# Performance work log

Measured on AMD Instinct MI355X. Metric: run time of the kernel, lower is better.

The kernel has to match this reference:

```python
import jax, jax.numpy as jnp
import numpy as np

B, C, H, W = 2, 64, 48, 48
NH = 8
EPS = 1e-5


def conv2d(x, w, b=None, pad=0):
    out = jax.lax.conv_general_dilated(x, w, (1, 1), [(pad, pad), (pad, pad)],
                                       dimension_numbers=('NCHW', 'OIHW', 'NCHW'))
    return out if b is None else out + b[None, :, None, None]


def bn2d(x, g, b, m, v):
    # eval-mode BatchNorm2d with running stats
    return (x - m[None, :, None, None]) * (g / jnp.sqrt(v + EPS))[None, :, None, None] + b[None, :, None, None]


def ln(x, g, b):
    mu = x.mean(-1, keepdims=True)
    var = ((x - mu) ** 2).mean(-1, keepdims=True)
    return (x - mu) / jnp.sqrt(var + EPS) * g + b


def _forward(x, y, pconv_w, pconv_b, bnd_g, bnd_b, bnd_m, bnd_v,
             lnx_g, lnx_b, lny_g, lny_b, lnz_g, lnz_b,
             k_w, k_b, qv_w, qv_b, proj_w, proj_b,
             c2w1, c2b1, c2bn1_g, c2bn1_b, c2bn1_m, c2bn1_v,
             c2w2, c2b2, c2bn2_g, c2bn2_b, c2bn2_m, c2bn2_v,
             bn2_g, bn2_b, bn2_m, bn2_v,
             f1w, fbn1_g, fbn1_b, fbn1_m, fbn1_v,
             f2w, fbn2_g, fbn2_b, fbn2_m, fbn2_v,
             f3w, f3b):
    Bq, Cq, Hq, Wq = x.shape
    N = Hq * Wq
    hd = Cq // NH
    scale = hd ** -0.5
    xy = conv2d(jnp.concatenate([x, y], 1), pconv_w, pconv_b, pad=0)
    xb = bn2d(x, bnd_g, bnd_b, bnd_m, bnd_v)
    yb = bn2d(y, bnd_g, bnd_b, bnd_m, bnd_v)
    xyb = bn2d(xy, bnd_g, bnd_b, bnd_m, bnd_v)
    sc1 = xb.reshape(Bq, Cq, N).transpose(0, 2, 1)  # [B,N,C]
    sd1 = yb.reshape(Bq, Cq, N).transpose(0, 2, 1)
    xl = ln(sc1, lnx_g, lnx_b)
    yl = ln(sd1, lny_g, lny_b)
    zl = ln(xyb.reshape(Bq, Cq, N).transpose(0, 2, 1), lnz_g, lnz_b)

    def qv_heads(t):
        qv = (t @ qv_w.T + qv_b).reshape(Bq, N, 2, NH, hd)
        return qv[:, :, 0].transpose(0, 2, 1, 3), qv[:, :, 1].transpose(0, 2, 1, 3)

    x_q, x_v = qv_heads(xl)
    y_q, y_v = qv_heads(yl)
    k = (zl @ k_w.T + k_b).reshape(Bq, N, NH, hd).transpose(0, 2, 1, 3)  # [B,H,N,hd]
    attn1 = jnp.einsum('bhnd,bhmd->bhnm', x_q, k) * scale
    attn2 = jnp.einsum('bhnd,bhmd->bhnm', y_q, k) * scale
    attn = jax.nn.softmax(attn1 * attn2, axis=-1)  # product of two score maps
    xo = jnp.einsum('bhnm,bhmd->bhnd', attn, x_v).transpose(0, 2, 1, 3).reshape(Bq, N, Cq) @ proj_w.T + proj_b
    yo = jnp.einsum('bhnm,bhmd->bhnd', attn, y_v).transpose(0, 2, 1, 3).reshape(Bq, N, Cq) @ proj_w.T + proj_b
    xo = (xo + sc1).transpose(0, 2, 1).reshape(Bq, Cq, Hq, Wq)
    yo = (yo + sd1).transpose(0, 2, 1).reshape(Bq, Cq, Hq, Wq)

    def conv2_block(t):  # shared-weight conv2 applied to both branches
        h = jax.nn.relu(bn2d(conv2d(t, c2w1, c2b1, pad=1), c2bn1_g, c2bn1_b, c2bn1_m, c2bn1_v))
        return jax.nn.relu(bn2d(conv2d(h, c2w2, c2b2, pad=1), c2bn2_g, c2bn2_b, c2bn2_m, c2bn2_v))

    xo = conv2_block(xo) + xo
    yo = conv2_block(yo) + yo
    cat = jnp.concatenate([xo + yo, xo * yo], 1)  # [B,2C,H,W]
    f = bn2d(cat, bn2_g, bn2_b, bn2_m, bn2_v)
    f = jax.nn.relu(bn2d(conv2d(f, f1w, None, pad=1), fbn1_g, fbn1_b, fbn1_m, fbn1_v))
    f = jax.nn.relu(bn2d(conv2d(f, f2w, None, pad=1), fbn2_g, fbn2_b, fbn2_m, fbn2_v))
    f = conv2d(f, f3w, f3b, pad=0)
    return cat + f


def setup_inputs() -> dict:
    ks = iter(jax.random.split(jax.random.key(0), 64))

    def nrm(shape, s=0.05):
        return jax.random.normal(next(ks), shape, jnp.float32) * s

    def bn_params(c):
        return (1.0 + nrm((c,)), nrm((c,)), nrm((c,)),
                jax.random.uniform(next(ks), (c,), jnp.float32, 0.5, 1.5))

    d = {}
    d['x'] = jax.random.normal(next(ks), (B, C, H, W), jnp.float32)
    d['y'] = jax.random.normal(next(ks), (B, C, H, W), jnp.float32)
    d['pconv_w'] = nrm((C, 2 * C, 1, 1)); d['pconv_b'] = nrm((C,))
    d['bnd_g'], d['bnd_b'], d['bnd_m'], d['bnd_v'] = bn_params(C)
    d['lnx_g'] = 1.0 + nrm((C,)); d['lnx_b'] = nrm((C,))
    d['lny_g'] = 1.0 + nrm((C,)); d['lny_b'] = nrm((C,))
    d['lnz_g'] = 1.0 + nrm((C,)); d['lnz_b'] = nrm((C,))
    d['k_w'] = nrm((C, C)); d['k_b'] = nrm((C,))
    d['qv_w'] = nrm((2 * C, C)); d['qv_b'] = nrm((2 * C,))
    d['proj_w'] = nrm((C, C)); d['proj_b'] = nrm((C,))
    d['c2w1'] = nrm((C, C, 3, 3)); d['c2b1'] = nrm((C,))
    d['c2bn1_g'], d['c2bn1_b'], d['c2bn1_m'], d['c2bn1_v'] = bn_params(C)
    d['c2w2'] = nrm((C, C, 3, 3)); d['c2b2'] = nrm((C,))
    d['c2bn2_g'], d['c2bn2_b'], d['c2bn2_m'], d['c2bn2_v'] = bn_params(C)
    d['bn2_g'], d['bn2_b'], d['bn2_m'], d['bn2_v'] = bn_params(2 * C)
    d['f1w'] = nrm((2 * C, 2 * C, 3, 3))
    d['fbn1_g'], d['fbn1_b'], d['fbn1_m'], d['fbn1_v'] = bn_params(2 * C)
    d['f2w'] = nrm((2 * C, 2 * C, 3, 3))
    d['fbn2_g'], d['fbn2_b'], d['fbn2_m'], d['fbn2_v'] = bn_params(2 * C)
    d['f3w'] = nrm((2 * C, 2 * C, 1, 1)); d['f3b'] = nrm((2 * C,))
    return d


def reference(x, y, pconv_w, pconv_b, bnd_g, bnd_b, bnd_m, bnd_v,
              lnx_g, lnx_b, lny_g, lny_b, lnz_g, lnz_b,
              k_w, k_b, qv_w, qv_b, proj_w, proj_b,
              c2w1, c2b1, c2bn1_g, c2bn1_b, c2bn1_m, c2bn1_v,
              c2w2, c2b2, c2bn2_g, c2bn2_b, c2bn2_m, c2bn2_v,
              bn2_g, bn2_b, bn2_m, bn2_v,
              f1w, fbn1_g, fbn1_b, fbn1_m, fbn1_v,
              f2w, fbn2_g, fbn2_b, fbn2_m, fbn2_v,
              f3w, f3b):
    return _forward(x, y, pconv_w, pconv_b, bnd_g, bnd_b, bnd_m, bnd_v,
                    lnx_g, lnx_b, lny_g, lny_b, lnz_g, lnz_b,
                    k_w, k_b, qv_w, qv_b, proj_w, proj_b,
                    c2w1, c2b1, c2bn1_g, c2bn1_b, c2bn1_m, c2bn1_v,
                    c2w2, c2b2, c2bn2_g, c2bn2_b, c2bn2_m, c2bn2_v,
                    bn2_g, bn2_b, bn2_m, bn2_v,
                    f1w, fbn1_g, fbn1_b, fbn1_m, fbn1_v,
                    f2w, fbn2_g, fbn2_b, fbn2_m, fbn2_v,
                    f3w, f3b)
```

## Files before the change

kernel.cpp:

```cpp
#include <hip/hip_runtime.h>
#include <hip/hip_bf16.h>

#define B_   2
#define C_   64
#define H_   48
#define W_   48
#define N_   (H_*W_)
#define NH_  8
#define HD_  8
#define EPS_ 1e-5f
#define S2_  0.125f
#define LOG2E_ 1.44269504f
#define FS_  (S2_ * LOG2E_)
#define S_   ((size_t)B_ * C_ * N_)
#define CN_  ((size_t)C_ * N_)
#define XTSZ_ ((size_t)(N_ + 2 * W_) * 128)
#define XTSC_ ((size_t)(N_ + 2 * W_) * 64)
#define PREB_ (B_ * N_ / 16)

typedef unsigned short u16;
typedef __attribute__((ext_vector_type(8))) short short8v;
typedef __attribute__((ext_vector_type(4))) float f32x4;
union F8 { uint4 u4; short8v s; unsigned int w[4]; };

__device__ __forceinline__ float wsum64(float v) {
#pragma unroll
  for (int o = 32; o > 0; o >>= 1) v += __shfl_xor(v, o, 64);
  return v;
}

__device__ __forceinline__ float ln_val(float t, float g, float b) {
  float mu  = wsum64(t) * (1.0f / 64.0f);
  float d   = t - mu;
  float var = wsum64(d * d) * (1.0f / 64.0f);
  return d * rsqrtf(var + EPS_) * g + b;
}

__device__ __forceinline__ u16 f2bf(float x) {
  union { float f; unsigned int u; } a; a.f = x;
  unsigned int r = a.u + 0x7fffu + ((a.u >> 16) & 1u);
  return (u16)(r >> 16);
}

__global__ __launch_bounds__(1024) void k_pre(
    const float* __restrict__ x, const float* __restrict__ y,
    const float* __restrict__ pw, const float* __restrict__ pb,
    const float* g, const float* bb, const float* m, const float* v,
    const float* lnxg, const float* lnxb,
    const float* lnyg, const float* lnyb,
    const float* lnzg, const float* lnzb,
    float* __restrict__ xl, float* __restrict__ yl, float* __restrict__ zl,
    const float* __restrict__ w1, const float* __restrict__ w2,
    const float* __restrict__ cw1, const float* __restrict__ cw2,
    const float* __restrict__ w3, const float* __restrict__ pjw,
    u16* __restrict__ wbo) {
  __shared__ float4 pwT[32][64];
  __shared__ float xs[16][64], ys[16][64];
  if (blockIdx.x >= PREB_) {
    int idx = (blockIdx.x - PREB_) * 1024 + threadIdx.x;
    if (idx >= 389120) return;
    if (idx < 294912) {
      int layer = idx / 147456, rem = idx - layer * 147456;
      int t = rem / 16384, r2 = rem - t * 16384;
      int co = r2 >> 7, ci = r2 & 127;
      wbo[idx] = f2bf((layer ? w2 : w1)[(size_t)co * 1152 + ci * 9 + t]);
    } else if (idx < 368640) {
      int k = idx - 294912;
      int layer = k / 36864, rem = k - layer * 36864;
      int t = rem / 4096, r2 = rem - t * 4096;
      int co = r2 >> 6, ci = r2 & 63;
      wbo[idx] = f2bf((layer ? cw2 : cw1)[(size_t)co * 576 + ci * 9 + t]);
    } else if (idx < 385024) {
      wbo[idx] = f2bf(w3[idx - 368640]);
    } else {
      wbo[idx] = f2bf(pjw[idx - 385024]);
    }
    return;
  }
  int w = threadIdx.x >> 6, c = threadIdx.x & 63;
  for (int idx = threadIdx.x; idx < 2048; idx += 1024) {
    int cc = idx & 63, i4 = idx >> 6;
    pwT[i4][cc] = *(const float4*)(pw + (size_t)cc * 2 * C_ + i4 * 4);
  }
  int row = blockIdx.x * 16 + w;
  int b = row / N_, n = row % N_;
  float xv = x[(size_t)(b * C_ + c) * N_ + n];
  float yv = y[(size_t)(b * C_ + c) * N_ + n];
  xs[w][c] = xv; ys[w][c] = yv;
  __syncthreads();
  const float4* xw = (const float4*)xs[w];
  const float4* yw = (const float4*)ys[w];
  float acc = pb[c];
#pragma unroll
  for (int t = 0; t < 16; ++t) {
    float4 a = xw[t], wv = pwT[t][c];
    acc += a.x * wv.x + a.y * wv.y + a.z * wv.z + a.w * wv.w;
  }
#pragma unroll
  for (int t = 0; t < 16; ++t) {
    float4 a = yw[t], wv = pwT[16 + t][c];
    acc += a.x * wv.x + a.y * wv.y + a.z * wv.z + a.w * wv.w;
  }
  float s  = g[c] * rsqrtf(v[c] + EPS_);
  float sh = bb[c] - m[c] * s;
  float tx = xv * s + sh;
  xl[(size_t)row * C_ + c] = ln_val(tx, lnxg[c], lnxb[c]);
  float ty = yv * s + sh;
  yl[(size_t)row * C_ + c] = ln_val(ty, lnyg[c], lnyb[c]);
  float tz = acc * s + sh;
  zl[(size_t)row * C_ + c] = ln_val(tz, lnzg[c], lnzb[c]);
}

__global__ __launch_bounds__(64) void k_qvk(
    const float* __restrict__ xl, const float* __restrict__ yl,
    const float* __restrict__ zl,
    const float* __restrict__ qvw, const float* __restrict__ qvb,
    const float* __restrict__ kw, const float* __restrict__ kb,
    u16* __restrict__ qxb, u16* __restrict__ qyb,
    u16* __restrict__ kbf, u16* __restrict__ vt) {
  int l = threadIdx.x;
  int part = blockIdx.y >> 2;
  int j0 = (blockIdx.y & 3) * 16;
  int row = blockIdx.x * 64 + l;
  int b = row / N_, n = row % N_;
  const float* inp = (part < 2) ? xl : (part < 4) ? yl : zl;
  float4 in[16];
  const float4* ir = (const float4*)(inp + (size_t)row * C_);
#pragma unroll
  for (int t = 0; t < 16; ++t) in[t] = ir[t];

  const float* wb   = (part == 4) ? kw : qvw;
  const float* bias = (part == 4) ? kb : qvb;
  int joff = (part == 1 || part == 3) ? 64 : 0;

  if (part == 1 || part == 3) {
    int vbase = (part == 1) ? 0 : 8;
#pragma unroll
    for (int jj = 0; jj < 16; ++jj) {
      int j = j0 + jj;
      const float4* wr = (const float4*)(wb + (size_t)(joff + j) * C_);
      float acc = bias[joff + j];
#pragma unroll
      for (int t = 0; t < 16; ++t) {
        float4 a = in[t], wv = wr[t];
        acc += a.x * wv.x + a.y * wv.y + a.z * wv.z + a.w * wv.w;
      }
      int h = j >> 3, d = j & 7;
      vt[((size_t)((b * NH_ + h) * 16 + vbase + d)) * N_ + n] = f2bf(acc);
    }
  } else {
    u16* dst = (part == 0) ? qxb : (part == 2) ? qyb : kbf;
#pragma unroll
    for (int gg = 0; gg < 2; ++gg) {
      int h = (j0 >> 3) + gg;
      union { uint4 u4; u16 s[8]; } pk;
#pragma unroll
      for (int d = 0; d < 8; ++d) {
        int j = h * 8 + d;
        const float4* wr = (const float4*)(wb + (size_t)(joff + j) * C_);
        float acc = bias[joff + j];
#pragma unroll
        for (int t = 0; t < 16; ++t) {
          float4 a = in[t], wv = wr[t];
          acc += a.x * wv.x + a.y * wv.y + a.z * wv.z + a.w * wv.w;
        }
        if (part == 0) acc *= FS_;
        pk.s[d] = f2bf(acc);
      }
      *(uint4*)(dst + ((size_t)(b * NH_ + h) * N_ + n) * 8) = pk.u4;
    }
  }
}

__global__ __launch_bounds__(128, 5) void k_attn8(
    const u16* __restrict__ qx, const u16* __restrict__ qy,
    const u16* __restrict__ kk, const u16* __restrict__ vt,
    u16* __restrict__ outx, u16* __restrict__ outy) {
  __shared__ float sAcc[2][4][64];
  __shared__ float sL[2][16];
  int qt = blockIdx.x, bh = blockIdx.y;
  int tid = threadIdx.x;
  int lane = tid & 63;
  int wave = tid >> 6;
  int l15 = lane & 15;
  int q0 = qt * 16;

  F8 qxf, qyf;
  size_t qoff = ((size_t)bh * N_ + q0 + l15) * 8;
  qxf.u4 = *(const uint4*)(qx + qoff);
  qyf.u4 = *(const uint4*)(qy + qoff);
  if (lane >= 16) {
    qxf.u4 = make_uint4(0u, 0u, 0u, 0u);
    qyf.u4 = make_uint4(0u, 0u, 0u, 0u);
  }

  int key0 = wave * (N_ / 2);
  const uint4* kp = (const uint4*)(kk + (size_t)bh * N_ * 8) + key0 + l15;
  const uint4* vp = (const uint4*)(vt + ((size_t)bh * 16 + l15) * N_ + key0)
                    + (lane >> 4);
  int addr0 = (((lane >> 4) & 1) * 32 + l15) * 4;
  int addr1 = addr0 + 64;
  int thi = lane >> 5;

  f32x4 acc0 = {0.f, 0.f, 0.f, 0.f};
  f32x4 acc1 = {0.f, 0.f, 0.f, 0.f};
  const f32x4 z4 = {0.f, 0.f, 0.f, 0.f};
  float lsum = 0.f;

  F8 ka, kb2, vf;
  ka.u4 = kp[0]; kb2.u4 = kp[16]; vf.u4 = *vp;
  for (int c = 0; c < 36; ++c) {
    F8 kaC = ka, kbC = kb2, vfC = vf;
    kp += 32; vp += 4;
    ka.u4 = kp[0]; kb2.u4 = kp[16]; vf.u4 = *vp;

    f32x4 s1a = __builtin_amdgcn_mfma_f32_16x16x32_bf16(kaC.s, qxf.s, z4, 0, 0, 0);
    f32x4 s2a = __builtin_amdgcn_mfma_f32_16x16x32_bf16(kaC.s, qyf.s, z4, 0, 0, 0);
    f32x4 s1b = __builtin_amdgcn_mfma_f32_16x16x32_bf16(kbC.s, qxf.s, z4, 0, 0, 0);
    f32x4 s2b = __builtin_amdgcn_mfma_f32_16x16x32_bf16(kbC.s, qyf.s, z4, 0, 0, 0);

    float p00 = exp2f(s1a[0] * s2a[0]), p01 = exp2f(s1a[1] * s2a[1]);
    float p02 = exp2f(s1a[2] * s2a[2]), p03 = exp2f(s1a[3] * s2a[3]);
    float p10 = exp2f(s1b[0] * s2b[0]), p11 = exp2f(s1b[1] * s2b[1]);
    float p12 = exp2f(s1b[2] * s2b[2]), p13 = exp2f(s1b[3] * s2b[3]);
    lsum += ((p00 + p01) + (p02 + p03)) + ((p10 + p11) + (p12 + p13));

    unsigned int pk00, pk10, pk01, pk11;
    asm("v_cvt_pk_bf16_f32 %0, %1, %2" : "=v"(pk00) : "v"(p00), "v"(p01));
    asm("v_cvt_pk_bf16_f32 %0, %1, %2" : "=v"(pk10) : "v"(p02), "v"(p03));
    asm("v_cvt_pk_bf16_f32 %0, %1, %2" : "=v"(pk01) : "v"(p10), "v"(p11));
    asm("v_cvt_pk_bf16_f32 %0, %1, %2" : "=v"(pk11) : "v"(p12), "v"(p13));

    int b00 = __builtin_amdgcn_ds_bpermute(addr0, (int)pk00);
    int b01 = __builtin_amdgcn_ds_bpermute(addr0, (int)pk01);
    int b10 = __builtin_amdgcn_ds_bpermute(addr0, (int)pk10);
    int b11 = __builtin_amdgcn_ds_bpermute(addr0, (int)pk11);
    int c00 = __builtin_amdgcn_ds_bpermute(addr1, (int)pk00);
    int c01 = __builtin_amdgcn_ds_bpermute(addr1, (int)pk01);
    int c10 = __builtin_amdgcn_ds_bpermute(addr1, (int)pk10);
    int c11 = __builtin_amdgcn_ds_bpermute(addr1, (int)pk11);

    F8 pf;
    pf.w[0] = (unsigned int)(thi ? b01 : b00);
    pf.w[1] = (unsigned int)(thi ? b11 : b10);
    pf.w[2] = (unsigned int)(thi ? c01 : c00);
    pf.w[3] = (unsigned int)(thi ? c11 : c10);
    if (c & 1)
      acc1 = __builtin_amdgcn_mfma_f32_16x16x32_bf16(pf.s, vfC.s, acc1, 0, 0, 0);
    else
      acc0 = __builtin_amdgcn_mfma_f32_16x16x32_bf16(pf.s, vfC.s, acc0, 0, 0, 0);
  }
  f32x4 acc = acc0 + acc1;

  lsum += __shfl_xor(lsum, 16, 64);
  lsum += __shfl_xor(lsum, 32, 64);
  if (lane < 16) sL[wave][lane] = lsum;
#pragma unroll
  for (int r = 0; r < 4; ++r) sAcc[wave][r][lane] = acc[r];
  __syncthreads();
  if (wave == 0) {
    float Linv = 1.f / (sL[0][l15] + sL[1][l15]);
    int b = bh >> 3, h = bh & 7;
    int d = l15 & 7;
    u16* ob = (l15 < 8) ? outx : outy;
    size_t cbase = (size_t)b * N_ * C_ + (size_t)h * 8 + d;
#pragma unroll
    for (int r = 0; r < 4; ++r) {
      int qrow = 4 * (lane >> 4) + r;
      float li = __shfl(Linv, qrow, 64);
      float a = sAcc[0][r][lane] + sAcc[1][r][lane];
      ob[cbase + (size_t)(q0 + qrow) * C_] = f2bf(a * li);
    }
  }
}

__global__ __launch_bounds__(64) void k_projm(
    const u16* __restrict__ attx, const u16* __restrict__ atty,
    const float* __restrict__ x, const float* __restrict__ y,
    const float* bg, const float* bb2, const float* bm, const float* bv,
    const u16* __restrict__ pwb, const float* __restrict__ pbias,
    float* __restrict__ xo4, u16* __restrict__ xt0) {
  if (blockIdx.x == 0) {
    int tg = (blockIdx.z * 4 + blockIdx.y) * 64 + threadIdx.x;
#pragma unroll
    for (int i = tg; i < 12288; i += 1024) {
      int img = i / 3072, r2 = i - img * 3072;
      int hi = r2 / 1536, o = r2 - hi * 1536;
      ((unsigned int*)(xt0 + (size_t)img * XTSC_
                       + (hi ? (size_t)(W_ + N_) * 64 : 0)))[o] = 0u;
    }
  }
  int l = threadIdx.x;
  int c = l & 15, gg = l >> 4;
  int px0 = blockIdx.x * 16;
  int ct0 = blockIdx.y * 16;
  int z = blockIdx.z;
  int branch = z >> 1, b = z & 1;
  const u16* att = (branch ? atty : attx) + (size_t)b * N_ * 64;
  const u16* aw = pwb + (size_t)(ct0 + c) * 64 + gg * 8;
  const f32x4 z4 = {0.f, 0.f, 0.f, 0.f};
  f32x4 acc0, acc1;
  {
    F8 af, bf;
    af.u4 = *(const uint4*)(aw);
    bf.u4 = *(const uint4*)(att + (size_t)(px0 + c) * 64 + gg * 8);
    acc0 = __builtin_amdgcn_mfma_f32_16x16x32_bf16(af.s, bf.s, z4, 0, 0, 0);
  }
  {
    F8 af, bf;
    af.u4 = *(const uint4*)(aw + 32);
    bf.u4 = *(const uint4*)(att + (size_t)(px0 + c) * 64 + 32 + gg * 8);
    acc1 = __builtin_amdgcn_mfma_f32_16x16x32_bf16(af.s, bf.s, z4, 0, 0, 0);
  }
  f32x4 acc = acc0 + acc1;
  int px = px0 + c;
  const float* xin = branch ? y : x;
#pragma unroll
  for (int r = 0; r < 4; ++r) {
    int cout = ct0 + 4 * gg + r;
    float s  = bg[cout] * rsqrtf(bv[cout] + EPS_);
    float sh = bb2[cout] - bm[cout] * s;
    float rr = xin[((size_t)b * C_ + cout) * N_ + px];
    float vv = acc[r] + pbias[cout] + rr * s + sh;
    xo4[(size_t)z * CN_ + (size_t)cout * N_ + px] = vv;
    xt0[(size_t)z * XTSC_ + (size_t)(W_ + px) * 64 + cout] = f2bf(vv);
  }
}

__global__ void k_catbn(const float* __restrict__ o2,
                        const float* __restrict__ g, const float* __restrict__ b2,
                        const float* __restrict__ m, const float* __restrict__ v,
                        float* __restrict__ cat, u16* __restrict__ xt1,
                        u16* __restrict__ xtf2) {
  int t = blockIdx.x * 256 + threadIdx.x;
  if (t < 12288) {
    int img = t / 6144, r2 = t - img * 6144;
    int hi = r2 / 3072, o = r2 - hi * 3072;
    ((unsigned int*)(xtf2 + (size_t)img * XTSZ_
                     + (hi ? (size_t)(W_ + N_) * 128 : 0)))[o] = 0u;
  } else if (t < 24576) {
    int i = t - 12288;
    int img = i / 6144, r2 = i - img * 6144;
    int hi = r2 / 3072, o = r2 - hi * 3072;
    ((unsigned int*)(xt1 + (size_t)img * XTSZ_
                     + (hi ? (size_t)(W_ + N_) * 128 : 0)))[o] = 0u;
  }
  int p4 = t * 4;
  int n  = p4 % N_;
  int c2 = (p4 / N_) % (2 * C_);
  int b  = p4 / (2 * C_ * N_);
  int c  = c2 & 63;
  float4 X = *(const float4*)(o2 + (size_t)b * CN_ + (size_t)c * N_ + n);
  float4 Y = *(const float4*)(o2 + (size_t)(2 + b) * CN_ + (size_t)c * N_ + n);
  float4 val;
  if (c2 < C_) val = make_float4(X.x + Y.x, X.y + Y.y, X.z + Y.z, X.w + Y.w);
  else         val = make_float4(X.x * Y.x, X.y * Y.y, X.z * Y.z, X.w * Y.w);
  size_t co = ((size_t)b * 2 * C_ + c2) * N_ + n;
  *(float4*)(cat + co) = val;
  float s  = g[c2] * rsqrtf(v[c2] + EPS_);
  float sh = b2[c2] - m[c2] * s;
  u16* xb = xt1 + (size_t)b * XTSZ_ + (size_t)(W_ + n) * 128 + c2;
  xb[0]   = f2bf(val.x * s + sh);
  xb[128] = f2bf(val.y * s + sh);
  xb[256] = f2bf(val.z * s + sh);
  xb[384] = f2bf(val.w * s + sh);
}

template<int MODE>
__global__ __launch_bounds__(64) void k_fmma(
    const u16* __restrict__ xt, const u16* __restrict__ wb,
    const float* __restrict__ cbias,
    const float* g, const float* b2, const float* m, const float* v,
    const float* __restrict__ resid,
    u16* __restrict__ xto, float* __restrict__ fo) {
  constexpr int CIN  = (MODE >= 2) ? 64 : 128;
  constexpr int NCB  = CIN / 32;
  constexpr int COUT = (MODE >= 2) ? 64 : 128;
  constexpr int TS   = CIN * COUT;
  constexpr size_t XTS = (size_t)(N_ + 2 * W_) * CIN;
  constexpr size_t XTSO = (size_t)(N_ + 2 * W_) * COUT;
  if (MODE == 2 && blockIdx.x == 0) {
    int tg = (blockIdx.z * 4 + blockIdx.y) * 64 + threadIdx.x;
#pragma unroll
    for (int i = tg; i < 12288; i += 1024) {
      int img = i / 3072, r2 = i - img * 3072;
      int hi = r2 / 1536, o = r2 - hi * 1536;
      ((unsigned int*)(xto + (size_t)img * XTSO
                       + (hi ? (size_t)(W_ + N_) * COUT : 0)))[o] = 0u;
    }
  }
  int l = threadIdx.x;
  int c = l & 15, gg = l >> 4;
  int px0 = blockIdx.x * 16;
  int ct0 = blockIdx.y * 16;
  int b = blockIdx.z;
  int x0 = px0 % W_;
  bool mL = (x0 == 0) && (c == 0);
  bool mR = (x0 == 32) && (c == 15);
  const u16* xb = xt + (size_t)b * XTS + (size_t)W_ * CIN;
  const u16* aw = wb + (size_t)(ct0 + c) * CIN + gg * 8;

  f32x4 acc0 = {0.f, 0.f, 0.f, 0.f};
  f32x4 acc1 = {0.f, 0.f, 0.f, 0.f};
#pragma unroll
  for (int cb = 0; cb < NCB; ++cb) {
#pragma unroll
    for (int t = 0; t < 9; ++t) {
      const int dx = t % 3 - 1, dy = t / 3 - 1;
      F8 af, bf;
      af.u4 = *(const uint4*)(aw + t * TS + cb * 32);
      int px = px0 + c + dx + dy * W_;
      px = max(px, -W_);
      bf.u4 = *(const uint4*)(xb + (ptrdiff_t)px * CIN + cb * 32 + gg * 8);
      bool msk = (dx < 0 && mL) || (dx > 0 && mR);
      if (msk) bf.u4 = make_uint4(0u, 0u, 0u, 0u);
      if ((t ^ cb) & 1)
        acc1 = __builtin_amdgcn_mfma_f32_16x16x32_bf16(af.s, bf.s, acc1, 0, 0, 0);
      else
        acc0 = __builtin_amdgcn_mfma_f32_16x16x32_bf16(af.s, bf.s, acc0, 0, 0, 0);
    }
  }
  f32x4 acc = acc0 + acc1;
  int px = px0 + c;
  if (MODE == 0 || MODE == 2) {
    union { ushort4 u; u16 s[4]; } pk;
#pragma unroll
    for (int r = 0; r < 4; ++r) {
      int cout = ct0 + 4 * gg + r;
      float a = acc[r] + (MODE == 2 ? cbias[cout] : 0.f);
      float s = g[cout] * rsqrtf(v[cout] + EPS_);
      float sh = b2[cout] - m[cout] * s;
      pk.s[r] = f2bf(fmaxf(a * s + sh, 0.f));
    }
    *(ushort4*)(xto + (size_t)b * XTSO + (size_t)(W_ + px) * COUT
                + ct0 + 4 * gg) = pk.u;
  } else {
#pragma unroll
    for (int r = 0; r < 4; ++r) {
      int cout = ct0 + 4 * gg + r;
      float a = acc[r] + cbias[cout];
      float s = g[cout] * rsqrtf(v[cout] + EPS_);
      float sh = b2[cout] - m[cout] * s;
      size_t off = (size_t)b * CN_ + (size_t)cout * N_ + px;
      fo[off] = fmaxf(a * s + sh, 0.f) + resid[off];
    }
  }
}

__global__ __launch_bounds__(64) void k_f3mma(
    const u16* __restrict__ xt3, const u16* __restrict__ w3b,
    const float* __restrict__ f3b, const float* __restrict__ cat,
    float* __restrict__ out) {
  int l = threadIdx.x;
  int c = l & 15, gg = l >> 4;
  int px0 = blockIdx.x * 16;
  int ct0 = blockIdx.y * 16;
  int b = blockIdx.z;
  const u16* xb = xt3 + (size_t)b * XTSZ_ + (size_t)W_ * 128;
  const u16* aw = w3b + (size_t)(ct0 + c) * 128 + gg * 8;
  f32x4 acc0 = {0.f, 0.f, 0.f, 0.f};
  f32x4 acc1 = {0.f, 0.f, 0.f, 0.f};
#pragma unroll
  for (int cb = 0; cb < 4; ++cb) {
    F8 af, bf;
    af.u4 = *(const uint4*)(aw + cb * 32);
    bf.u4 = *(const uint4*)(xb + (size_t)(px0 + c) * 128 + cb * 32 + gg * 8);
    if (cb & 1)
      acc1 = __builtin_amdgcn_mfma_f32_16x16x32_bf16(af.s, bf.s, acc1, 0, 0, 0);
    else
      acc0 = __builtin_amdgcn_mfma_f32_16x16x32_bf16(af.s, bf.s, acc0, 0, 0, 0);
  }
  f32x4 acc = acc0 + acc1;
  int px = px0 + c;
#pragma unroll
  for (int r = 0; r < 4; ++r) {
    int cout = ct0 + 4 * gg + r;
    size_t off = ((size_t)b * 2 * C_ + cout) * N_ + px;
    out[off] = acc[r] + f3b[cout] + cat[off];
  }
}

extern "C" void kernel_launch(void* const* d_in, const int* in_sizes, int n_in,
                              void* d_out, int out_size, void* d_ws, size_t ws_size,
                              hipStream_t stream) {
  const float* x       = (const float*)d_in[0];
  const float* y       = (const float*)d_in[1];
  const float* pconv_w = (const float*)d_in[2];
  const float* pconv_b = (const float*)d_in[3];
  const float* bnd_g = (const float*)d_in[4];
  const float* bnd_b = (const float*)d_in[5];
  const float* bnd_m = (const float*)d_in[6];
  const float* bnd_v = (const float*)d_in[7];
  const float* lnx_g = (const float*)d_in[8];
  const float* lnx_b = (const float*)d_in[9];
  const float* lny_g = (const float*)d_in[10];
  const float* lny_b = (const float*)d_in[11];
  const float* lnz_g = (const float*)d_in[12];
  const float* lnz_b = (const float*)d_in[13];
  const float* k_w   = (const float*)d_in[14];
  const float* k_b   = (const float*)d_in[15];
  const float* qv_w  = (const float*)d_in[16];
  const float* qv_b  = (const float*)d_in[17];
  const float* proj_w = (const float*)d_in[18];
  const float* proj_b = (const float*)d_in[19];
  const float* c2w1  = (const float*)d_in[20];
  const float* c2b1  = (const float*)d_in[21];
  const float* c2bn1_g = (const float*)d_in[22];
  const float* c2bn1_b = (const float*)d_in[23];
  const float* c2bn1_m = (const float*)d_in[24];
  const float* c2bn1_v = (const float*)d_in[25];
  const float* c2w2  = (const float*)d_in[26];
  const float* c2b2  = (const float*)d_in[27];
  const float* c2bn2_g = (const float*)d_in[28];
  const float* c2bn2_b = (const float*)d_in[29];
  const float* c2bn2_m = (const float*)d_in[30];
  const float* c2bn2_v = (const float*)d_in[31];
  const float* bn2_g = (const float*)d_in[32];
  const float* bn2_b = (const float*)d_in[33];
  const float* bn2_m = (const float*)d_in[34];
  const float* bn2_v = (const float*)d_in[35];
  const float* f1w   = (const float*)d_in[36];
  const float* fbn1_g = (const float*)d_in[37];
  const float* fbn1_b = (const float*)d_in[38];
  const float* fbn1_m = (const float*)d_in[39];
  const float* fbn1_v = (const float*)d_in[40];
  const float* f2w   = (const float*)d_in[41];
  const float* fbn2_g = (const float*)d_in[42];
  const float* fbn2_b = (const float*)d_in[43];
  const float* fbn2_m = (const float*)d_in[44];
  const float* fbn2_v = (const float*)d_in[45];
  const float* f3w   = (const float*)d_in[46];
  const float* f3b   = (const float*)d_in[47];

  float* ws = (float*)d_ws;
  float* sl1 = ws + 1 * S_;
  float* sl2 = ws + 2 * S_;
  float* sl3 = ws + 3 * S_;
  u16* attx = (u16*)(ws + 1 * S_);
  u16* atty = attx + (size_t)B_ * N_ * 64;
  u16* xtC0 = (u16*)(ws + 5 * S_);
  u16* xtC1 = (u16*)ws;
  u16* xtF1 = (u16*)(ws + 5 * S_ / 4);
  u16* xtF2 = (u16*)ws;
  u16* xt3  = (u16*)(ws + 5 * S_ / 4);
  float* xo4 = ws + 3 * S_;
  float* o2  = ws + 5 * S_;
  float* cat = ws + 3 * S_;
  u16* wb   = (u16*)(ws + 7 * S_);
  u16* wbf1 = wb;
  u16* wbf2 = wb + 147456;
  u16* wbc1 = wb + 294912;
  u16* wbc2 = wb + 331776;
  u16* wb3  = wb + 368640;
  u16* wbp  = wb + 385024;

  k_pre<<<PREB_ + 380, 1024, 0, stream>>>(x, y, pconv_w, pconv_b,
                                    bnd_g, bnd_b, bnd_m, bnd_v,
                                    lnx_g, lnx_b, lny_g, lny_b, lnz_g, lnz_b,
                                    sl1, sl2, sl3,
                                    f1w, f2w, c2w1, c2w2, f3w, proj_w, wb);
  u16* qxb = (u16*)(ws + 4 * S_);
  u16* qyb = qxb + (size_t)B_ * NH_ * N_ * 8;
  u16* kbf = (u16*)(ws + 5 * S_);
  u16* vtb = (u16*)(ws + 6 * S_);
  {
    dim3 g(B_ * N_ / 64, 20);
    k_qvk<<<g, 64, 0, stream>>>(sl1, sl2, sl3, qv_w, qv_b, k_w, k_b,
                                qxb, qyb, kbf, vtb);
  }
  {
    dim3 g(N_ / 16, B_ * NH_);
    k_attn8<<<g, 128, 0, stream>>>(qxb, qyb, kbf, vtb, attx, atty);
  }
  {
    dim3 g(N_ / 16, 4, 4);
    k_projm<<<g, 64, 0, stream>>>(attx, atty, x, y,
                                  bnd_g, bnd_b, bnd_m, bnd_v,
                                  wbp, proj_b, xo4, xtC0);
  }
  {
    dim3 g(N_ / 16, 4, 4);
    k_fmma<2><<<g, 64, 0, stream>>>(xtC0, wbc1, c2b1,
        c2bn1_g, c2bn1_b, c2bn1_m, c2bn1_v, nullptr, xtC1, nullptr);
  }
  {
    dim3 g(N_ / 16, 4, 4);
    k_fmma<3><<<g, 64, 0, stream>>>(xtC1, wbc2, c2b2,
        c2bn2_g, c2bn2_b, c2bn2_m, c2bn2_v, xo4, nullptr, o2);
  }
  k_catbn<<<576, 256, 0, stream>>>(o2, bn2_g, bn2_b, bn2_m, bn2_v,
                                   cat, xtF1, xtF2);
  {
    dim3 g(N_ / 16, 8, B_);
    k_fmma<0><<<g, 64, 0, stream>>>(xtF1, wbf1, nullptr,
        fbn1_g, fbn1_b, fbn1_m, fbn1_v, nullptr, xtF2, nullptr);
    k_fmma<0><<<g, 64, 0, stream>>>(xtF2, wbf2, nullptr,
        fbn2_g, fbn2_b, fbn2_m, fbn2_v, nullptr, xt3, nullptr);
  }
  {
    dim3 g(N_ / 16, 8, B_);
    k_f3mma<<<g, 64, 0, stream>>>(xt3, wb3, f3b, cat, (float*)d_out);
  }
}
```

Baseline: 297.1 us.

## Split attention keys across four waves and unroll the chunk loop by two

The attention kernel now uses 256-thread blocks, and each of the four waves handles a quarter of the keys instead of a half. The per-wave partial sums and row normalizers are combined through shared memory at the end. The main loop is unrolled by two, with a separate prefetch register set for each chunk to hide load latency. This halves the serial key chain per wave and adds latency hiding, at the cost of more registers, more reduction work and a higher launch-bound block size.

```diff
diff --git a/kernel.cpp b/kernel.cpp
--- a/kernel.cpp
+++ b/kernel.cpp
@@ -17,6 +17,7 @@
 #define XTSZ_ ((size_t)(N_ + 2 * W_) * 128)
 #define XTSC_ ((size_t)(N_ + 2 * W_) * 64)
 #define PREB_ (B_ * N_ / 16)
+#define AWV_ 4
 
 typedef unsigned short u16;
 typedef __attribute__((ext_vector_type(8))) short short8v;
@@ -172,12 +173,44 @@
   }
 }
 
-__global__ __launch_bounds__(128, 5) void k_attn8(
+#define ATT_CHUNK(KA, KB, VF, ACC)                                          \
+  {                                                                         \
+    f32x4 s1a = __builtin_amdgcn_mfma_f32_16x16x32_bf16(KA.s, qxf.s, z4, 0, 0, 0); \
+    f32x4 s2a = __builtin_amdgcn_mfma_f32_16x16x32_bf16(KA.s, qyf.s, z4, 0, 0, 0); \
+    f32x4 s1b = __builtin_amdgcn_mfma_f32_16x16x32_bf16(KB.s, qxf.s, z4, 0, 0, 0); \
+    f32x4 s2b = __builtin_amdgcn_mfma_f32_16x16x32_bf16(KB.s, qyf.s, z4, 0, 0, 0); \
+    float p00 = exp2f(s1a[0] * s2a[0]), p01 = exp2f(s1a[1] * s2a[1]);       \
+    float p02 = exp2f(s1a[2] * s2a[2]), p03 = exp2f(s1a[3] * s2a[3]);       \
+    float p10 = exp2f(s1b[0] * s2b[0]), p11 = exp2f(s1b[1] * s2b[1]);       \
+    float p12 = exp2f(s1b[2] * s2b[2]), p13 = exp2f(s1b[3] * s2b[3]);       \
+    lsum += ((p00 + p01) + (p02 + p03)) + ((p10 + p11) + (p12 + p13));      \
+    unsigned int pk00, pk10, pk01, pk11;                                    \
+    asm("v_cvt_pk_bf16_f32 %0, %1, %2" : "=v"(pk00) : "v"(p00), "v"(p01));  \
+    asm("v_cvt_pk_bf16_f32 %0, %1, %2" : "=v"(pk10) : "v"(p02), "v"(p03));  \
+    asm("v_cvt_pk_bf16_f32 %0, %1, %2" : "=v"(pk01) : "v"(p10), "v"(p11));  \
+    asm("v_cvt_pk_bf16_f32 %0, %1, %2" : "=v"(pk11) : "v"(p12), "v"(p13));  \
+    int b00 = __builtin_amdgcn_ds_bpermute(addr0, (int)pk00);               \
+    int b01 = __builtin_amdgcn_ds_bpermute(addr0, (int)pk01);               \
+    int b10 = __builtin_amdgcn_ds_bpermute(addr0, (int)pk10);               \
+    int b11 = __builtin_amdgcn_ds_bpermute(addr0, (int)pk11);               \
+    int c00 = __builtin_amdgcn_ds_bpermute(addr1, (int)pk00);               \
+    int c01 = __builtin_amdgcn_ds_bpermute(addr1, (int)pk01);               \
+    int c10 = __builtin_amdgcn_ds_bpermute(addr1, (int)pk10);               \
+    int c11 = __builtin_amdgcn_ds_bpermute(addr1, (int)pk11);               \
+    F8 pf;                                                                  \
+    pf.w[0] = (unsigned int)(thi ? b01 : b00);                              \
+    pf.w[1] = (unsigned int)(thi ? b11 : b10);                              \
+    pf.w[2] = (unsigned int)(thi ? c01 : c00);                              \
+    pf.w[3] = (unsigned int)(thi ? c11 : c10);                              \
+    ACC = __builtin_amdgcn_mfma_f32_16x16x32_bf16(pf.s, VF.s, ACC, 0, 0, 0);\
+  }
+
+__global__ __launch_bounds__(256, 4) void k_attn9(
     const u16* __restrict__ qx, const u16* __restrict__ qy,
     const u16* __restrict__ kk, const u16* __restrict__ vt,
     u16* __restrict__ outx, u16* __restrict__ outy) {
-  __shared__ float sAcc[2][4][64];
-  __shared__ float sL[2][16];
+  __shared__ float sAcc[AWV_][4][64];
+  __shared__ float sL[AWV_][16];
   int qt = blockIdx.x, bh = blockIdx.y;
   int tid = threadIdx.x;
   int lane = tid & 63;
@@ -194,7 +227,7 @@
     qyf.u4 = make_uint4(0u, 0u, 0u, 0u);
   }
 
-  int key0 = wave * (N_ / 2);
+  int key0 = wave * (N_ / AWV_);
   const uint4* kp = (const uint4*)(kk + (size_t)bh * N_ * 8) + key0 + l15;
   const uint4* vp = (const uint4*)(vt + ((size_t)bh * 16 + l15) * N_ + key0)
                     + (lane >> 4);
@@ -207,48 +240,15 @@
   const f32x4 z4 = {0.f, 0.f, 0.f, 0.f};
   float lsum = 0.f;
 
-  F8 ka, kb2, vf;
-  ka.u4 = kp[0]; kb2.u4 = kp[16]; vf.u4 = *vp;
-  for (int c = 0; c < 36; ++c) {
-    F8 kaC = ka, kbC = kb2, vfC = vf;
-    kp += 32; vp += 4;
-    ka.u4 = kp[0]; kb2.u4 = kp[16]; vf.u4 = *vp;
-
-    f32x4 s1a = __builtin_amdgcn_mfma_f32_16x16x32_bf16(kaC.s, qxf.s, z4, 0, 0, 0);
-    f32x4 s2a = __builtin_amdgcn_mfma_f32_16x16x32_bf16(kaC.s, qyf.s, z4, 0, 0, 0);
-    f32x4 s1b = __builtin_amdgcn_mfma_f32_16x16x32_bf16(kbC.s, qxf.s, z4, 0, 0, 0);
-    f32x4 s2b = __builtin_amdgcn_mfma_f32_16x16x32_bf16(kbC.s, qyf.s, z4, 0, 0, 0);
-
-    float p00 = exp2f(s1a[0] * s2a[0]), p01 = exp2f(s1a[1] * s2a[1]);
-    float p02 = exp2f(s1a[2] * s2a[2]), p03 = exp2f(s1a[3] * s2a[3]);
-    float p10 = exp2f(s1b[0] * s2b[0]), p11 = exp2f(s1b[1] * s2b[1]);
-    float p12 = exp2f(s1b[2] * s2b[2]), p13 = exp2f(s1b[3] * s2b[3]);
-    lsum += ((p00 + p01) + (p02 + p03)) + ((p10 + p11) + (p12 + p13));
-
-    unsigned int pk00, pk10, pk01, pk11;
-    asm("v_cvt_pk_bf16_f32 %0, %1, %2" : "=v"(pk00) : "v"(p00), "v"(p01));
-    asm("v_cvt_pk_bf16_f32 %0, %1, %2" : "=v"(pk10) : "v"(p02), "v"(p03));
-    asm("v_cvt_pk_bf16_f32 %0, %1, %2" : "=v"(pk01) : "v"(p10), "v"(p11));
-    asm("v_cvt_pk_bf16_f32 %0, %1, %2" : "=v"(pk11) : "v"(p12), "v"(p13));
-
-    int b00 = __builtin_amdgcn_ds_bpermute(addr0, (int)pk00);
-    int b01 = __builtin_amdgcn_ds_bpermute(addr0, (int)pk01);
-    int b10 = __builtin_amdgcn_ds_bpermute(addr0, (int)pk10);
-    int b11 = __builtin_amdgcn_ds_bpermute(addr0, (int)pk11);
-    int c00 = __builtin_amdgcn_ds_bpermute(addr1, (int)pk00);
-    int c01 = __builtin_amdgcn_ds_bpermute(addr1, (int)pk01);
-    int c10 = __builtin_amdgcn_ds_bpermute(addr1, (int)pk10);
-    int c11 = __builtin_amdgcn_ds_bpermute(addr1, (int)pk11);
-
-    F8 pf;
-    pf.w[0] = (unsigned int)(thi ? b01 : b00);
-    pf.w[1] = (unsigned int)(thi ? b11 : b10);
-    pf.w[2] = (unsigned int)(thi ? c01 : c00);
-    pf.w[3] = (unsigned int)(thi ? c11 : c10);
-    if (c & 1)
-      acc1 = __builtin_amdgcn_mfma_f32_16x16x32_bf16(pf.s, vfC.s, acc1, 0, 0, 0);
-    else
-      acc0 = __builtin_amdgcn_mfma_f32_16x16x32_bf16(pf.s, vfC.s, acc0, 0, 0, 0);
+  F8 ka0, kb0, vf0, ka1, kb1, vf1;
+  ka0.u4 = kp[0];  kb0.u4 = kp[16]; vf0.u4 = vp[0];
+  ka1.u4 = kp[32]; kb1.u4 = kp[48]; vf1.u4 = vp[4];
+  for (int c = 0; c < N_ / AWV_ / 32; c += 2) {
+    ATT_CHUNK(ka0, kb0, vf0, acc0);
+    ka0.u4 = kp[64]; kb0.u4 = kp[80]; vf0.u4 = vp[8];
+    ATT_CHUNK(ka1, kb1, vf1, acc1);
+    kp += 64; vp += 8;
+    ka1.u4 = kp[32]; kb1.u4 = kp[48]; vf1.u4 = vp[4];
   }
   f32x4 acc = acc0 + acc1;
 
@@ -259,7 +259,10 @@
   for (int r = 0; r < 4; ++r) sAcc[wave][r][lane] = acc[r];
   __syncthreads();
   if (wave == 0) {
-    float Linv = 1.f / (sL[0][l15] + sL[1][l15]);
+    float L = 0.f;
+#pragma unroll
+    for (int w2 = 0; w2 < AWV_; ++w2) L += sL[w2][l15];
+    float Linv = 1.f / L;
     int b = bh >> 3, h = bh & 7;
     int d = l15 & 7;
     u16* ob = (l15 < 8) ? outx : outy;
@@ -268,7 +271,9 @@
     for (int r = 0; r < 4; ++r) {
       int qrow = 4 * (lane >> 4) + r;
       float li = __shfl(Linv, qrow, 64);
-      float a = sAcc[0][r][lane] + sAcc[1][r][lane];
+      float a = 0.f;
+#pragma unroll
+      for (int w2 = 0; w2 < AWV_; ++w2) a += sAcc[w2][r][lane];
       ob[cbase + (size_t)(q0 + qrow) * C_] = f2bf(a * li);
     }
   }
@@ -570,7 +575,7 @@
   }
   {
     dim3 g(N_ / 16, B_ * NH_);
-    k_attn8<<<g, 128, 0, stream>>>(qxb, qyb, kbf, vtb, attx, atty);
+    k_attn9<<<g, 256, 0, stream>>>(qxb, qyb, kbf, vtb, attx, atty);
   }
   {
     dim3 g(N_ / 16, 4, 4);
```

After: 294.7 us. Within noise of the previous version (-0.8%).
